# Optimization experiments

Hardware: AMD Instinct MI355X
Metric: run time of the kernel (lower is better)

## Reference

```python
import jax, jax.numpy as jnp
import numpy as np

B, T, C = 2, 2048, 1024
NH = 16
HD = C // NH
SCALE = 1.0 / np.sqrt(HD).astype(np.float32)


def setup_inputs() -> dict:
    key = jax.random.key(0)
    k1, k2, k3 = jax.random.split(key, 3)
    x = jax.random.normal(k1, (B, T, C), dtype=jnp.float32)
    # torch Linear stores weight (out,in) and computes x @ W^T; we store the
    # transposed (in,out) layout directly, scaled like default init.
    w_qkv = jax.random.normal(k2, (C, 3 * C), dtype=jnp.float32) * (1.0 / np.sqrt(C))
    w_proj = jax.random.normal(k3, (C, C), dtype=jnp.float32) * (1.0 / np.sqrt(C))
    return {"x": x, "w_qkv": w_qkv, "w_proj": w_proj}


def reference(x, w_qkv, w_proj):
    b, t, c = x.shape
    qkv = x @ w_qkv                                  # (b, t, 3c)
    q, k, v = jnp.split(qkv, 3, axis=-1)
    q = q.reshape(b, t, NH, HD)
    k = k.reshape(b, t, NH, HD)
    v = v.reshape(b, t, NH, HD)
    # scores: (b, nh, t, t) — full materialization, faithful to the original
    att = jnp.einsum("bthd,bshd->bhts", q, k) * SCALE
    causal = jnp.tril(jnp.ones((t, t), dtype=bool))  # (t, t)
    neg = jnp.finfo(att.dtype).min
    att = jnp.where(causal[None, None, :, :], att, neg)
    weights = jax.nn.softmax(att, axis=-1)
    y = jnp.einsum("bhts,bshd->bthd", weights, v).reshape(b, t, c)
    y = y @ w_proj
    return y
```

## Files before the change

### kernel.cpp

```cpp
#include <hip/hip_runtime.h>
#include <hip/hip_bf16.h>
#include <stdint.h>

typedef __bf16 bf16x8 __attribute__((ext_vector_type(8)));
typedef float f32x4 __attribute__((ext_vector_type(4)));
typedef unsigned short us4v __attribute__((ext_vector_type(4)));
typedef unsigned short us8v __attribute__((ext_vector_type(8)));

#define B_   2
#define T_   2048
#define C_   1024
#define NH_  16
#define HD_  64

__device__ __forceinline__ unsigned short f2bf(float f) {
  unsigned int u = __builtin_bit_cast(unsigned int, f);
  u += 0x7fffu + ((u >> 16) & 1u);
  return (unsigned short)(u >> 16);
}
__device__ __forceinline__ float bf2f(unsigned short u) {
  unsigned int x = ((unsigned int)u) << 16;
  return __builtin_bit_cast(float, x);
}

__device__ __forceinline__ void gload16(const void* g, void* l) {
  __builtin_amdgcn_global_load_lds(
      (const __attribute__((address_space(1))) unsigned int*)g,
      (__attribute__((address_space(3))) unsigned int*)l, 16, 0, 0);
}

__device__ __forceinline__ f32x4 mfma16(bf16x8 a, bf16x8 b, f32x4 c) {
  return __builtin_amdgcn_mfma_f32_16x16x32_bf16(a, b, c, 0, 0, 0);
}

__global__ __launch_bounds__(256) void cast_x_kernel(const float4* __restrict__ in,
                                                     us4v* __restrict__ out) {
  int i = blockIdx.x * 256 + threadIdx.x;
  float4 f = in[i];
  us4v o; o[0] = f2bf(f.x); o[1] = f2bf(f.y); o[2] = f2bf(f.z); o[3] = f2bf(f.w);
  out[i] = o;
}

__global__ __launch_bounds__(256) void transpose_cast_kernel(const float* __restrict__ w,
                                                             unsigned short* __restrict__ wT,
                                                             int K, int N) {
  __shared__ float tile[32][33];
  int n0 = blockIdx.x * 32, k0 = blockIdx.y * 32;
  int tx = threadIdx.x, ty = threadIdx.y;
  #pragma unroll
  for (int i = 0; i < 4; ++i)
    tile[ty + 8*i][tx] = w[(size_t)(k0 + ty + 8*i) * N + n0 + tx];
  __syncthreads();
  #pragma unroll
  for (int i = 0; i < 4; ++i)
    wT[(size_t)(n0 + ty + 8*i) * K + k0 + tx] = f2bf(tile[tx][ty + 8*i]);
}

__device__ __forceinline__ void gemm_core(const unsigned short* __restrict__ A,
                                          const unsigned short* __restrict__ Bt,
                                          int K, int m0, int n0,
                                          unsigned short* lA, unsigned short* lB,
                                          f32x4 acc[4][4]) {
  const int t = threadIdx.x;
  const int lane = t & 63, w = t >> 6;
  const int wm = w >> 1, wn = w & 1;
  const int g = lane >> 4, r16 = lane & 15;
  #pragma unroll
  for (int i = 0; i < 4; ++i)
    #pragma unroll
    for (int j = 0; j < 4; ++j) acc[i][j] = (f32x4){0.f, 0.f, 0.f, 0.f};

  for (int k0 = 0; k0 < K; k0 += 64) {
    #pragma unroll
    for (int i = 0; i < 4; ++i) {
      int slot = i * 256 + t;
      int r = slot >> 3, p = slot & 7;
      int q = p ^ (r & 7);
      gload16(A  + (size_t)(m0 + r) * K + k0 + q * 8, lA + slot * 8);
      gload16(Bt + (size_t)(n0 + r) * K + k0 + q * 8, lB + slot * 8);
    }
    asm volatile("s_waitcnt vmcnt(0)" ::: "memory");
    __syncthreads();

    bf16x8 af[4][2], bfr[4][2];
    #pragma unroll
    for (int mi = 0; mi < 4; ++mi)
      #pragma unroll
      for (int kk = 0; kk < 2; ++kk) {
        int r = wm * 64 + mi * 16 + r16;
        int ps = (kk * 4 + g) ^ (r & 7);
        af[mi][kk] = *(const bf16x8*)(lA + r * 64 + ps * 8);
      }
    #pragma unroll
    for (int ni = 0; ni < 4; ++ni)
      #pragma unroll
      for (int kk = 0; kk < 2; ++kk) {
        int r = wn * 64 + ni * 16 + r16;
        int ps = (kk * 4 + g) ^ (r & 7);
        bfr[ni][kk] = *(const bf16x8*)(lB + r * 64 + ps * 8);
      }
    #pragma unroll
    for (int mi = 0; mi < 4; ++mi)
      #pragma unroll
      for (int ni = 0; ni < 4; ++ni)
        #pragma unroll
        for (int kk = 0; kk < 2; ++kk)
          acc[mi][ni] = mfma16(af[mi][kk], bfr[ni][kk], acc[mi][ni]);
    __syncthreads();
  }
}

__device__ __forceinline__ int xcd_swz(int flat, int nwg) {
  int cpx = nwg >> 3;
  return (flat & 7) * cpx + (flat >> 3);
}

__global__ __launch_bounds__(256) void gemm_qkv_kernel(const unsigned short* __restrict__ xb,
                                                       const unsigned short* __restrict__ wT,
                                                       unsigned short* __restrict__ qb,
                                                       unsigned short* __restrict__ kb,
                                                       unsigned short* __restrict__ vb) {
  __shared__ unsigned short lA[128 * 64];
  __shared__ unsigned short lB[128 * 64];
  f32x4 acc[4][4];
  const int nbx = 3 * C_ / 128;
  int flat = xcd_swz(blockIdx.y * nbx + blockIdx.x, nbx * ((B_ * T_) / 128));
  const int m0 = (flat / nbx) * 128, n0 = (flat % nbx) * 128;
  gemm_core(xb, wT, C_, m0, n0, lA, lB, acc);
  const int t = threadIdx.x, lane = t & 63, w = t >> 6;
  const int wm = w >> 1, wn = w & 1, g = lane >> 4, r16 = lane & 15;
  #pragma unroll
  for (int mi = 0; mi < 4; ++mi)
    #pragma unroll
    for (int ni = 0; ni < 4; ++ni)
      #pragma unroll
      for (int j = 0; j < 4; ++j) {
        int gm = m0 + wm * 64 + mi * 16 + g * 4 + j;
        int gn = n0 + wn * 64 + ni * 16 + r16;
        int b = gm >> 11, tt = gm & 2047;
        int s = gn >> 10, rem = gn & 1023;
        int h = rem >> 6, d = rem & 63;
        unsigned short val = f2bf(acc[mi][ni][j]);
        size_t idx = ((size_t)(b * NH_ + h) * T_ + tt) * HD_ + d;
        if (s == 0)      qb[idx] = val;
        else if (s == 1) kb[idx] = val;
        else             vb[idx] = val;
      }
}

__global__ __launch_bounds__(256) void gemm_proj_kernel(const unsigned short* __restrict__ ab,
                                                        const unsigned short* __restrict__ wT,
                                                        float* __restrict__ out) {
  __shared__ unsigned short lA[128 * 64];
  __shared__ unsigned short lB[128 * 64];
  f32x4 acc[4][4];
  const int nbx = C_ / 128;
  int flat = xcd_swz(blockIdx.y * nbx + blockIdx.x, nbx * ((B_ * T_) / 128));
  const int m0 = (flat / nbx) * 128, n0 = (flat % nbx) * 128;
  gemm_core(ab, wT, C_, m0, n0, lA, lB, acc);
  const int t = threadIdx.x, lane = t & 63, w = t >> 6;
  const int wm = w >> 1, wn = w & 1, g = lane >> 4, r16 = lane & 15;
  #pragma unroll
  for (int mi = 0; mi < 4; ++mi)
    #pragma unroll
    for (int ni = 0; ni < 4; ++ni)
      #pragma unroll
      for (int j = 0; j < 4; ++j) {
        int gm = m0 + wm * 64 + mi * 16 + g * 4 + j;
        int gn = n0 + wn * 64 + ni * 16 + r16;
        out[(size_t)gm * C_ + gn] = acc[mi][ni][j];
      }
}

__global__ __launch_bounds__(256, 4) void attn_kernel(const unsigned short* __restrict__ qb,
                                                      const unsigned short* __restrict__ kb,
                                                      const unsigned short* __restrict__ vb,
                                                      unsigned short* __restrict__ ao,
                                                      unsigned short* __restrict__ partB,
                                                      float* __restrict__ mlbuf) {
  __shared__ unsigned short LDS[16384];
  const int bx = blockIdx.x, bh = blockIdx.y;
  int tile, kvLo, kvHi, mode;
  if (bx < 16)      { tile = 16 + bx; kvLo = 0;  kvHi = 16;       mode = 1; }
  else if (bx < 32) { tile = 47 - bx; kvLo = 16; kvHi = tile + 1; mode = 2; }
  else              { tile = 47 - bx; kvLo = 0;  kvHi = tile + 1; mode = 0; }
  const int qt0 = tile * 64;
  const int t = threadIdx.x, lane = t & 63, w4 = t >> 6;
  const int g = lane >> 4, r16 = lane & 15;

  const unsigned short* Q  = qb + (size_t)bh * (T_ * HD_);
  const unsigned short* Kp = kb + (size_t)bh * (T_ * HD_);
  const unsigned short* Vp = vb + (size_t)bh * (T_ * HD_);

  bf16x8 qf[2];
  {
    int qrow = qt0 + w4 * 16 + r16;
    #pragma unroll
    for (int kk = 0; kk < 2; ++kk) {
      us8v raw = *(const us8v*)(Q + (size_t)qrow * HD_ + kk * 32 + g * 8);
      bf16x8 qv;
      #pragma unroll
      for (int j = 0; j < 8; ++j) qv[j] = (__bf16)(bf2f(raw[j]) * 0.125f);
      qf[kk] = qv;
    }
  }

  f32x4 o[4];
  #pragma unroll
  for (int c = 0; c < 4; ++c) o[c] = (f32x4){0.f, 0.f, 0.f, 0.f};
  float mrun = -__builtin_inff(), lrun = 0.f;

  const int kr0 = t >> 3,         kp0 = (t & 7) ^ (kr0 & 7);
  const int kr1 = (t + 256) >> 3, kp1 = (t & 7) ^ (kr1 & 7);
  const int colp = (lane & 32) | ((lane & 12) << 1) | ((lane >> 2) & 4) | (lane & 3);
  const int cslot = colp >> 3, cwithin = colp & 7;

  gload16(Kp + (size_t)(kvLo * 64 + kr0) * HD_ + kp0 * 8, LDS + t * 8);
  gload16(Kp + (size_t)(kvLo * 64 + kr1) * HD_ + kp1 * 8, LDS + (t + 256) * 8);
  us8v nv0 = *(const us8v*)(Vp + (size_t)(kvLo * 64 + lane) * HD_ + w4 * 16);
  us8v nv1 = *(const us8v*)(Vp + (size_t)(kvLo * 64 + lane) * HD_ + w4 * 16 + 8);

  for (int it = kvLo; it < kvHi; ++it) {
    const int cur = (it - kvLo) & 1;
    const unsigned short* Kl = LDS + cur * 4096;
    unsigned short* Vt = LDS + 8192 + cur * 4096;

    asm volatile("s_waitcnt vmcnt(0)" ::: "memory");
    #pragma unroll
    for (int u = 0; u < 8; ++u) {
      int d = w4 * 16 + u;
      Vt[d * 64 + ((cslot ^ u) << 3) + cwithin] = nv0[u];
    }
    #pragma unroll
    for (int u = 0; u < 8; ++u) {
      int d = w4 * 16 + 8 + u;
      Vt[d * 64 + ((cslot ^ u) << 3) + cwithin] = nv1[u];
    }
    __syncthreads();

    if (it + 1 < kvHi) {
      const int kv0n = (it + 1) * 64;
      unsigned short* Kn = LDS + (cur ^ 1) * 4096;
      gload16(Kp + (size_t)(kv0n + kr0) * HD_ + kp0 * 8, Kn + t * 8);
      gload16(Kp + (size_t)(kv0n + kr1) * HD_ + kp1 * 8, Kn + (t + 256) * 8);
      nv0 = *(const us8v*)(Vp + (size_t)(kv0n + lane) * HD_ + w4 * 16);
      nv1 = *(const us8v*)(Vp + (size_t)(kv0n + lane) * HD_ + w4 * 16 + 8);
    }

    {
      f32x4 s4t[4];
      #pragma unroll
      for (int c = 0; c < 4; ++c) s4t[c] = (f32x4){0.f, 0.f, 0.f, 0.f};
      #pragma unroll
      for (int c = 0; c < 4; ++c)
        #pragma unroll
        for (int kk = 0; kk < 2; ++kk) {
          int r = c * 16 + r16;
          int ps = (kk * 4 + g) ^ (r & 7);
          bf16x8 kf = *(const bf16x8*)(Kl + r * 64 + ps * 8);
          s4t[c] = mfma16(kf, qf[kk], s4t[c]);
        }
      if (it == tile) {
        int qloc = w4 * 16 + r16;
        #pragma unroll
        for (int c = 0; c < 4; ++c)
          #pragma unroll
          for (int j = 0; j < 4; ++j)
            if (c * 16 + g * 4 + j > qloc) s4t[c][j] = -1e30f;
      }
      float mx = -1e30f;
      #pragma unroll
      for (int c = 0; c < 4; ++c)
        #pragma unroll
        for (int j = 0; j < 4; ++j) mx = fmaxf(mx, s4t[c][j]);
      mx = fmaxf(mx, __shfl_xor(mx, 16));
      mx = fmaxf(mx, __shfl_xor(mx, 32));
      float mn = fmaxf(mrun, mx);
      float alpha = __expf(mrun - mn);
      mrun = mn;
      float rs = 0.f;
      #pragma unroll
      for (int c = 0; c < 4; ++c)
        #pragma unroll
        for (int j = 0; j < 4; ++j) {
          float p = __expf(s4t[c][j] - mn);
          s4t[c][j] = p;
          rs += p;
        }
      rs += __shfl_xor(rs, 16);
      rs += __shfl_xor(rs, 32);
      lrun = lrun * alpha + rs;
      #pragma unroll
      for (int c = 0; c < 4; ++c)
        #pragma unroll
        for (int j = 0; j < 4; ++j) o[c][j] *= alpha;

      bf16x8 pf[2];
      #pragma unroll
      for (int kk = 0; kk < 2; ++kk) {
        bf16x8 p;
        #pragma unroll
        for (int j = 0; j < 4; ++j) {
          p[j]     = (__bf16)s4t[2 * kk][j];
          p[4 + j] = (__bf16)s4t[2 * kk + 1][j];
        }
        pf[kk] = p;
      }
      #pragma unroll
      for (int c = 0; c < 4; ++c) {
        int rv = c * 16 + r16;
        #pragma unroll
        for (int kk = 0; kk < 2; ++kk) {
          int slot = (4 * kk + g) ^ (r16 & 7);
          bf16x8 vf = *(const bf16x8*)(Vt + rv * 64 + slot * 8);
          o[c] = mfma16(vf, pf[kk], o[c]);
        }
      }
    }
  }

  if (mode && g == 0) {
    int prow = (bh * 16 + (tile - 16)) * 64 + w4 * 16 + r16;
    float* mlp = mlbuf + (size_t)prow * 4;
    if (mode == 1) { mlp[0] = mrun; mlp[1] = lrun; }
    else           { mlp[2] = mrun; mlp[3] = lrun; }
  }

  const int deadK = ((kvHi - kvLo - 1) & 1) ^ 1;
  unsigned short* ep = LDS + deadK * 4096 + w4 * 1024;
  float inv = 1.f / lrun;
  #pragma unroll
  for (int c = 0; c < 4; ++c) {
    us4v pk;
    #pragma unroll
    for (int j = 0; j < 4; ++j) pk[j] = f2bf(o[c][j] * inv);
    int slot = (4 * c + g) ^ r16;
    *(us4v*)(ep + r16 * 64 + slot * 4) = pk;
  }
  asm volatile("s_waitcnt lgkmcnt(0)" ::: "memory");
  __builtin_amdgcn_sched_barrier(0);
  {
    int q = lane >> 2, seg = lane & 3;
    us4v a0 = *(const us4v*)(ep + q * 64 + (((seg * 4 + 0) ^ q) & 15) * 4);
    us4v a1 = *(const us4v*)(ep + q * 64 + (((seg * 4 + 1) ^ q) & 15) * 4);
    us4v a2 = *(const us4v*)(ep + q * 64 + (((seg * 4 + 2) ^ q) & 15) * 4);
    us4v a3 = *(const us4v*)(ep + q * 64 + (((seg * 4 + 3) ^ q) & 15) * 4);
    us8v o0 = {a0[0],a0[1],a0[2],a0[3],a1[0],a1[1],a1[2],a1[3]};
    us8v o1 = {a2[0],a2[1],a2[2],a2[3],a3[0],a3[1],a3[2],a3[3]};
    if (mode != 2) {
      size_t rowg = (size_t)(bh >> 4) * T_ + qt0 + w4 * 16 + q;
      int colg = (bh & 15) * 64 + seg * 16;
      *(us8v*)(ao + rowg * C_ + colg)     = o0;
      *(us8v*)(ao + rowg * C_ + colg + 8) = o1;
    } else {
      size_t prow = (size_t)(bh * 16 + (tile - 16)) * 64 + w4 * 16 + q;
      *(us8v*)(partB + prow * 64 + seg * 16)     = o0;
      *(us8v*)(partB + prow * 64 + seg * 16 + 8) = o1;
    }
  }
}

__global__ __launch_bounds__(256) void attn_merge_kernel(unsigned short* __restrict__ ao,
                                                         const unsigned short* __restrict__ partB,
                                                         const float* __restrict__ mlbuf) {
  const int blk = blockIdx.x;
  const int bh = blk >> 4, ti = blk & 15;
  const int t = threadIdx.x;
  const int row = t >> 2, seg = t & 3;
  const size_t prow = (size_t)(bh * 16 + ti) * 64 + row;
  const float* mlp = mlbuf + prow * 4;
  float mA = mlp[0], lA = mlp[1], mB = mlp[2], lB = mlp[3];
  float m = fmaxf(mA, mB);
  float wA = lA * __expf(mA - m), wB = lB * __expf(mB - m);
  float rinv = 1.f / (wA + wB);
  wA *= rinv; wB *= rinv;
  size_t rowg = (size_t)(bh >> 4) * T_ + (16 + ti) * 64 + row;
  unsigned short* aop = ao + rowg * C_ + (bh & 15) * 64 + seg * 16;
  const unsigned short* obp = partB + prow * 64 + seg * 16;
  us8v oa0 = *(const us8v*)(aop);
  us8v oa1 = *(const us8v*)(aop + 8);
  us8v ob0 = *(const us8v*)(obp);
  us8v ob1 = *(const us8v*)(obp + 8);
  us8v r0, r1;
  #pragma unroll
  for (int j = 0; j < 8; ++j) {
    r0[j] = f2bf(bf2f(oa0[j]) * wA + bf2f(ob0[j]) * wB);
    r1[j] = f2bf(bf2f(oa1[j]) * wA + bf2f(ob1[j]) * wB);
  }
  *(us8v*)(aop)     = r0;
  *(us8v*)(aop + 8) = r1;
}

extern "C" void kernel_launch(void* const* d_in, const int* in_sizes, int n_in,
                              void* d_out, int out_size, void* d_ws, size_t ws_size,
                              hipStream_t stream) {
  const float* x      = (const float*)d_in[0];
  const float* w_qkv  = (const float*)d_in[1];
  const float* w_proj = (const float*)d_in[2];
  float* out = (float*)d_out;
  char* ws = (char*)d_ws;

  unsigned short* xb     = (unsigned short*)(ws);
  unsigned short* wqkvT  = (unsigned short*)(ws + 8388608);
  unsigned short* wprojT = (unsigned short*)(ws + 14680064);
  unsigned short* qb     = (unsigned short*)(ws + 16777216);
  unsigned short* kb     = (unsigned short*)(ws + 25165824);
  unsigned short* vb     = (unsigned short*)(ws + 33554432);
  unsigned short* ao     = xb;
  unsigned short* partB  = wqkvT;
  float*          mlbuf  = (float*)(ws + 8388608 + 4194304);

  cast_x_kernel<<<4096, 256, 0, stream>>>((const float4*)x, (us4v*)xb);
  transpose_cast_kernel<<<dim3(3 * C_ / 32, C_ / 32), dim3(32, 8), 0, stream>>>(
      w_qkv, wqkvT, C_, 3 * C_);
  transpose_cast_kernel<<<dim3(C_ / 32, C_ / 32), dim3(32, 8), 0, stream>>>(
      w_proj, wprojT, C_, C_);
  gemm_qkv_kernel<<<dim3(3 * C_ / 128, (B_ * T_) / 128), 256, 0, stream>>>(
      xb, wqkvT, qb, kb, vb);
  attn_kernel<<<dim3(48, 32), 256, 0, stream>>>(qb, kb, vb, ao, partB, mlbuf);
  attn_merge_kernel<<<512, 256, 0, stream>>>(ao, partB, mlbuf);
  gemm_proj_kernel<<<dim3(C_ / 128, (B_ * T_) / 128), 256, 0, stream>>>(
      ao, wprojT, out);
}
```

Baseline: 123.4 us.

## Triple-buffer K tiles with two-ahead prefetch, remap grid to XCDs, add setprio

Deepens the attention KV pipeline from double to triple buffering for K, with prefetch two iterations ahead and partial vmcnt waits. The aim is to hide more global-load latency behind the MFMA work. The grid is flattened to 1D and remapped so that each group of blocks sharing a head lands together, likely to improve L2 reuse across XCDs. s_setprio is raised around the MFMA sections. LDS use grows from 32KB to 40KB, which may reduce occupancy, and the extra V registers raise register pressure.

```diff
diff --git a/kernel.cpp b/kernel.cpp
--- a/kernel.cpp
+++ b/kernel.cpp
@@ -178,13 +178,17 @@
                                                       unsigned short* __restrict__ ao,
                                                       unsigned short* __restrict__ partB,
                                                       float* __restrict__ mlbuf) {
-  __shared__ unsigned short LDS[16384];
-  const int bx = blockIdx.x, bh = blockIdx.y;
+  __shared__ unsigned short LDS[20480];
+  const int L = blockIdx.x;
+  const int inner = L >> 3;
+  const int bh = (L & 7) * 4 + (inner / 48);
+  const int bx = inner % 48;
   int tile, kvLo, kvHi, mode;
   if (bx < 16)      { tile = 16 + bx; kvLo = 0;  kvHi = 16;       mode = 1; }
   else if (bx < 32) { tile = 47 - bx; kvLo = 16; kvHi = tile + 1; mode = 2; }
   else              { tile = 47 - bx; kvLo = 0;  kvHi = tile + 1; mode = 0; }
   const int qt0 = tile * 64;
+  const int len = kvHi - kvLo;
   const int t = threadIdx.x, lane = t & 63, w4 = t >> 6;
   const int g = lane >> 4, r16 = lane & 15;
 
@@ -217,40 +221,59 @@
 
   gload16(Kp + (size_t)(kvLo * 64 + kr0) * HD_ + kp0 * 8, LDS + t * 8);
   gload16(Kp + (size_t)(kvLo * 64 + kr1) * HD_ + kp1 * 8, LDS + (t + 256) * 8);
-  us8v nv0 = *(const us8v*)(Vp + (size_t)(kvLo * 64 + lane) * HD_ + w4 * 16);
-  us8v nv1 = *(const us8v*)(Vp + (size_t)(kvLo * 64 + lane) * HD_ + w4 * 16 + 8);
-
-  for (int it = kvLo; it < kvHi; ++it) {
-    const int cur = (it - kvLo) & 1;
-    const unsigned short* Kl = LDS + cur * 4096;
-    unsigned short* Vt = LDS + 8192 + cur * 4096;
-
-    asm volatile("s_waitcnt vmcnt(0)" ::: "memory");
-    #pragma unroll
-    for (int u = 0; u < 8; ++u) {
-      int d = w4 * 16 + u;
-      Vt[d * 64 + ((cslot ^ u) << 3) + cwithin] = nv0[u];
-    }
-    #pragma unroll
-    for (int u = 0; u < 8; ++u) {
-      int d = w4 * 16 + 8 + u;
-      Vt[d * 64 + ((cslot ^ u) << 3) + cwithin] = nv1[u];
+  us8v nvA0 = *(const us8v*)(Vp + (size_t)(kvLo * 64 + lane) * HD_ + w4 * 16);
+  us8v nvA1 = *(const us8v*)(Vp + (size_t)(kvLo * 64 + lane) * HD_ + w4 * 16 + 8);
+  us8v nvB0, nvB1;
+  if (len > 1) {
+    const int k1 = (kvLo + 1) * 64;
+    gload16(Kp + (size_t)(k1 + kr0) * HD_ + kp0 * 8, LDS + 4096 + t * 8);
+    gload16(Kp + (size_t)(k1 + kr1) * HD_ + kp1 * 8, LDS + 4096 + (t + 256) * 8);
+    nvB0 = *(const us8v*)(Vp + (size_t)(k1 + lane) * HD_ + w4 * 16);
+    nvB1 = *(const us8v*)(Vp + (size_t)(k1 + lane) * HD_ + w4 * 16 + 8);
+  }
+
+  for (int ii = 0; ii < len; ++ii) {
+    const int it = kvLo + ii;
+    const unsigned short* Kl = LDS + (ii % 3) * 4096;
+    unsigned short* Vt = LDS + 12288 + (ii & 1) * 4096;
+
+    if (ii + 1 < len) { asm volatile("s_waitcnt vmcnt(4)" ::: "memory"); }
+    else              { asm volatile("s_waitcnt vmcnt(0)" ::: "memory"); }
+    {
+      us8v v0, v1;
+      if (ii & 1) { v0 = nvB0; v1 = nvB1; } else { v0 = nvA0; v1 = nvA1; }
+      #pragma unroll
+      for (int u = 0; u < 8; ++u) {
+        int d = w4 * 16 + u;
+        Vt[d * 64 + ((cslot ^ u) << 3) + cwithin] = v0[u];
+      }
+      #pragma unroll
+      for (int u = 0; u < 8; ++u) {
+        int d = w4 * 16 + 8 + u;
+        Vt[d * 64 + ((cslot ^ u) << 3) + cwithin] = v1[u];
+      }
     }
     __syncthreads();
 
-    if (it + 1 < kvHi) {
-      const int kv0n = (it + 1) * 64;
-      unsigned short* Kn = LDS + (cur ^ 1) * 4096;
-      gload16(Kp + (size_t)(kv0n + kr0) * HD_ + kp0 * 8, Kn + t * 8);
-      gload16(Kp + (size_t)(kv0n + kr1) * HD_ + kp1 * 8, Kn + (t + 256) * 8);
-      nv0 = *(const us8v*)(Vp + (size_t)(kv0n + lane) * HD_ + w4 * 16);
-      nv1 = *(const us8v*)(Vp + (size_t)(kv0n + lane) * HD_ + w4 * 16 + 8);
+    if (ii + 2 < len) {
+      const int kn = (it + 2) * 64;
+      unsigned short* Kn = LDS + ((ii + 2) % 3) * 4096;
+      gload16(Kp + (size_t)(kn + kr0) * HD_ + kp0 * 8, Kn + t * 8);
+      gload16(Kp + (size_t)(kn + kr1) * HD_ + kp1 * 8, Kn + (t + 256) * 8);
+      if (ii & 1) {
+        nvB0 = *(const us8v*)(Vp + (size_t)(kn + lane) * HD_ + w4 * 16);
+        nvB1 = *(const us8v*)(Vp + (size_t)(kn + lane) * HD_ + w4 * 16 + 8);
+      } else {
+        nvA0 = *(const us8v*)(Vp + (size_t)(kn + lane) * HD_ + w4 * 16);
+        nvA1 = *(const us8v*)(Vp + (size_t)(kn + lane) * HD_ + w4 * 16 + 8);
+      }
     }
 
     {
       f32x4 s4t[4];
       #pragma unroll
       for (int c = 0; c < 4; ++c) s4t[c] = (f32x4){0.f, 0.f, 0.f, 0.f};
+      __builtin_amdgcn_s_setprio(1);
       #pragma unroll
       for (int c = 0; c < 4; ++c)
         #pragma unroll
@@ -260,6 +283,7 @@
           bf16x8 kf = *(const bf16x8*)(Kl + r * 64 + ps * 8);
           s4t[c] = mfma16(kf, qf[kk], s4t[c]);
         }
+      __builtin_amdgcn_s_setprio(0);
       if (it == tile) {
         int qloc = w4 * 16 + r16;
         #pragma unroll
@@ -306,6 +330,7 @@
         }
         pf[kk] = p;
       }
+      __builtin_amdgcn_s_setprio(1);
       #pragma unroll
       for (int c = 0; c < 4; ++c) {
         int rv = c * 16 + r16;
@@ -316,6 +341,7 @@
           o[c] = mfma16(vf, pf[kk], o[c]);
         }
       }
+      __builtin_amdgcn_s_setprio(0);
     }
   }
 
@@ -326,8 +352,7 @@
     else           { mlp[2] = mrun; mlp[3] = lrun; }
   }
 
-  const int deadK = ((kvHi - kvLo - 1) & 1) ^ 1;
-  unsigned short* ep = LDS + deadK * 4096 + w4 * 1024;
+  unsigned short* ep = LDS + (len % 3) * 4096 + w4 * 1024;
   float inv = 1.f / lrun;
   #pragma unroll
   for (int c = 0; c < 4; ++c) {
@@ -417,7 +442,7 @@
       w_proj, wprojT, C_, C_);
   gemm_qkv_kernel<<<dim3(3 * C_ / 128, (B_ * T_) / 128), 256, 0, stream>>>(
       xb, wqkvT, qb, kb, vb);
-  attn_kernel<<<dim3(48, 32), 256, 0, stream>>>(qb, kb, vb, ao, partB, mlbuf);
+  attn_kernel<<<dim3(1536), 256, 0, stream>>>(qb, kb, vb, ao, partB, mlbuf);
   attn_merge_kernel<<<512, 256, 0, stream>>>(ao, partB, mlbuf);
   gemm_proj_kernel<<<dim3(C_ / 128, (B_ * T_) / 128), 256, 0, stream>>>(
       ao, wprojT, out);
```

After: 124.9 us. No clear change (+1.2%).
